# Performance work log

Hardware: AMD Instinct MI355X
Metric: run time of the kernel (lower is better)

The kernel has to match this reference:

```python
import jax, jax.numpy as jnp
import numpy as np

B, T, E = 4, 2048, 1024
H = 16
HS = E // H  # head_size = d_model // num_heads, d_model == E here
D_FF = 4 * E
EPS = 1e-5


def _layernorm(x, g, b):
    mu = jnp.mean(x, axis=-1, keepdims=True)
    var = jnp.var(x, axis=-1, keepdims=True)
    return (x - mu) * jax.lax.rsqrt(var + EPS) * g + b


def setup_inputs() -> dict:
    key = jax.random.key(0)
    ks = jax.random.split(key, 12)
    s_e = 1.0 / np.sqrt(E)
    s_ff = 1.0 / np.sqrt(D_FF)
    return {
        "x": jax.random.normal(ks[0], (B, T, E), jnp.float32),
        "ln1_g": jnp.ones((E,), jnp.float32),
        "ln1_b": jnp.zeros((E,), jnp.float32),
        "Wq": jax.random.normal(ks[1], (E, E), jnp.float32) * s_e,
        "bq": jnp.zeros((E,), jnp.float32),
        "Wk": jax.random.normal(ks[2], (E, E), jnp.float32) * s_e,
        "bk": jnp.zeros((E,), jnp.float32),
        "Wv": jax.random.normal(ks[3], (E, E), jnp.float32) * s_e,
        "bv": jnp.zeros((E,), jnp.float32),
        "Wp": jax.random.normal(ks[4], (E, E), jnp.float32) * s_e,
        "bp": jnp.zeros((E,), jnp.float32),
        "ln2_g": jnp.ones((E,), jnp.float32),
        "ln2_b": jnp.zeros((E,), jnp.float32),
        "W1": jax.random.normal(ks[5], (E, D_FF), jnp.float32) * s_e,
        "b1": jnp.zeros((D_FF,), jnp.float32),
        "W2": jax.random.normal(ks[6], (D_FF, E), jnp.float32) * s_ff,
        "b2": jnp.zeros((E,), jnp.float32),
    }


def reference(x, ln1_g, ln1_b, Wq, bq, Wk, bk, Wv, bv, Wp, bp,
              ln2_g, ln2_b, W1, b1, W2, b2):
    # --- attention sublayer ---
    h = _layernorm(x, ln1_g, ln1_b)                      # [B,T,E]
    q = (h @ Wq + bq).reshape(B, T, H, HS)
    k = (h @ Wk + bk).reshape(B, T, H, HS)
    v = (h @ Wv + bv).reshape(B, T, H, HS)
    scores = jnp.einsum('bqhd,bkhd->bhqk', q, k) * (HS ** -0.5)  # [B,H,T,T]
    causal = jnp.tril(jnp.ones((T, T), bool))
    scores = jnp.where(causal, scores, -jnp.inf)
    w = jax.nn.softmax(scores, axis=-1)
    attn = jnp.einsum('bhqk,bkhd->bqhd', w, v).reshape(B, T, H * HS)
    x = x + attn @ Wp + bp
    # --- FFN sublayer ---
    h2 = _layernorm(x, ln2_g, ln2_b)
    x = x + jax.nn.relu(h2 @ W1 + b1) @ W2 + b2
    return x
```

## Files before the change

kernel.cpp:

```cpp
#include <hip/hip_runtime.h>
#include <hip/hip_bf16.h>

#define B_ 4
#define T_ 2048
#define E_ 1024
#define H_ 16
#define HS_ 64
#define DFF_ 4096
#define M_ (B_ * T_)
#define LDQ_ (3 * E_)

typedef __bf16 bf16_t;
typedef __bf16 bf16x4 __attribute__((ext_vector_type(4)));
typedef __bf16 bf16x8 __attribute__((ext_vector_type(8)));
typedef float f32x4 __attribute__((ext_vector_type(4)));

#define AS1 __attribute__((address_space(1)))
#define AS3 __attribute__((address_space(3)))

__device__ __forceinline__ void gload_lds16(const void* g, void* l) {
  __builtin_amdgcn_global_load_lds((AS1 void*)(g), (AS3 void*)(l), 16, 0, 0);
}

__global__ __launch_bounds__(256) void wtrans_kernel(
    const float* __restrict__ W, bf16_t* __restrict__ Wt, int Krows, int Ncols) {
  __shared__ float tile[32][33];
  int tx = threadIdx.x, ty = threadIdx.y;
  int n0 = blockIdx.x * 32, k0 = blockIdx.y * 32;
#pragma unroll
  for (int i = 0; i < 32; i += 8)
    tile[ty + i][tx] = W[(long)(k0 + ty + i) * Ncols + n0 + tx];
  __syncthreads();
#pragma unroll
  for (int i = 0; i < 32; i += 8)
    Wt[(long)(n0 + ty + i) * Krows + k0 + tx] = (bf16_t)tile[tx][ty + i];
}

__global__ __launch_bounds__(256) void bcat_kernel(const float* a, const float* b,
                                                   const float* c, float* o) {
  int i = blockIdx.x * 256 + threadIdx.x;
  o[i] = i < 1024 ? a[i] : (i < 2048 ? b[i - 1024] : c[i - 2048]);
}

__global__ __launch_bounds__(256) void layernorm_kernel(
    const float* __restrict__ in, const float* __restrict__ g,
    const float* __restrict__ b, bf16_t* __restrict__ out) {
  int row = blockIdx.x;
  int tid = threadIdx.x;
  const float4* inr = (const float4*)(in + (long)row * E_);
  float4 v = inr[tid];
  float s = v.x + v.y + v.z + v.w;
  float ss = v.x * v.x + v.y * v.y + v.z * v.z + v.w * v.w;
#pragma unroll
  for (int o = 32; o; o >>= 1) {
    s += __shfl_xor(s, o);
    ss += __shfl_xor(ss, o);
  }
  __shared__ float red[8];
  int wv = tid >> 6;
  if ((tid & 63) == 0) {
    red[wv] = s;
    red[4 + wv] = ss;
  }
  __syncthreads();
  s = red[0] + red[1] + red[2] + red[3];
  ss = red[4] + red[5] + red[6] + red[7];
  float mu = s * (1.f / E_);
  float var = ss * (1.f / E_) - mu * mu;
  float rs = rsqrtf(var + 1e-5f);
  int ci = tid * 4;
  float4 gv = *(const float4*)(g + ci);
  float4 bv = *(const float4*)(b + ci);
  long o0 = (long)row * E_ + ci;
  out[o0 + 0] = (bf16_t)((v.x - mu) * rs * gv.x + bv.x);
  out[o0 + 1] = (bf16_t)((v.y - mu) * rs * gv.y + bv.y);
  out[o0 + 2] = (bf16_t)((v.z - mu) * rs * gv.z + bv.z);
  out[o0 + 3] = (bf16_t)((v.w - mu) * rs * gv.w + bv.w);
}

template <int MODE>
__global__ __launch_bounds__(256, 2) void gemm_bt_kernel(
    const bf16_t* __restrict__ A, const bf16_t* __restrict__ Bt,
    const float* __restrict__ bias, const float* __restrict__ resid,
    void* __restrict__ out, int N, int K) {
  __shared__ bf16_t As[2][128 * 64];
  __shared__ bf16_t Bs[2][128 * 64];
  const int tid = threadIdx.x;
  const int lane = tid & 63;
  const int wave = tid >> 6;
  const int wr = wave >> 1, wc = wave & 1;
  const int quad = lane >> 4, l16 = lane & 15;
  const int id = blockIdx.y * gridDim.x + blockIdx.x;
  const int xcd = id & 7;
  const int k_ = id >> 3;
  const int bxr = k_ % gridDim.x;
  const int byr = (k_ / gridDim.x) * 8 + xcd;
  const long rowBase = (long)byr * 128;
  const long colBase = (long)bxr * 128;

  f32x4 acc[4][4] = {};

  auto stage = [&](int buf, int k0) {
#pragma unroll
    for (int i = 0; i < 4; ++i) {
      int c = i * 256 + tid;
      int row = c >> 3;
      int gcol = ((c & 7) ^ (row & 7)) * 8;
      gload_lds16(&A[(rowBase + row) * K + k0 + gcol],
                  &As[buf][(i * 256 + wave * 64) * 8]);
      gload_lds16(&Bt[(colBase + row) * K + k0 + gcol],
                  &Bs[buf][(i * 256 + wave * 64) * 8]);
    }
  };

  stage(0, 0);
  __syncthreads();

  for (int k0 = 0; k0 < K; k0 += 64) {
    const int cur = (k0 >> 6) & 1;
    if (k0 + 64 < K) stage(cur ^ 1, k0 + 64);
#pragma unroll
    for (int kk = 0; kk < 2; ++kk) {
      bf16x8 af[4], bfr[4];
#pragma unroll
      for (int i = 0; i < 4; ++i) {
        int rowA = wr * 64 + i * 16 + l16;
        af[i] = *(const bf16x8*)&As[cur][(rowA * 8 + ((quad + 4 * kk) ^ (rowA & 7))) * 8];
        int rowB = wc * 64 + i * 16 + l16;
        bfr[i] = *(const bf16x8*)&Bs[cur][(rowB * 8 + ((quad + 4 * kk) ^ (rowB & 7))) * 8];
      }
#pragma unroll
      for (int mi = 0; mi < 4; ++mi)
#pragma unroll
        for (int ni = 0; ni < 4; ++ni)
          acc[mi][ni] = __builtin_amdgcn_mfma_f32_16x16x32_bf16(
              af[mi], bfr[ni], acc[mi][ni], 0, 0, 0);
    }
    __syncthreads();
  }

#pragma unroll
  for (int mi = 0; mi < 4; ++mi) {
#pragma unroll
    for (int ni = 0; ni < 4; ++ni) {
      int colg = (int)colBase + wc * 64 + ni * 16 + l16;
      float bv = bias[colg];
#pragma unroll
      for (int r = 0; r < 4; ++r) {
        long rowg = rowBase + wr * 64 + mi * 16 + quad * 4 + r;
        float v = acc[mi][ni][r] + bv;
        long idx = rowg * N + colg;
        if (MODE == 0) {
          ((bf16_t*)out)[idx] = (bf16_t)v;
        } else if (MODE == 1) {
          ((float*)out)[idx] = v + resid[idx];
        } else {
          ((bf16_t*)out)[idx] = (bf16_t)fmaxf(v, 0.f);
        }
      }
    }
  }
}

__global__ __launch_bounds__(256) void vtrans_kernel(
    const bf16_t* __restrict__ qkv, bf16_t* __restrict__ vt) {
  __shared__ bf16_t tile[32][33];
  int tx = threadIdx.x, ty = threadIdx.y;
  int t0 = blockIdx.x * 32;
  int d0 = (blockIdx.y & 1) * 32;
  int bh = blockIdx.y >> 1;
  int b = bh >> 4, hh = bh & 15;
#pragma unroll
  for (int i = 0; i < 32; i += 8)
    tile[ty + i][tx] =
        qkv[(long)(b * T_ + t0 + ty + i) * LDQ_ + 2 * E_ + hh * HS_ + d0 + tx];
  __syncthreads();
#pragma unroll
  for (int i = 0; i < 32; i += 8)
    vt[((long)bh * HS_ + d0 + ty + i) * T_ + t0 + tx] = tile[tx][ty + i];
}

__global__ __launch_bounds__(256) void flash_attn_kernel(
    const bf16_t* __restrict__ qkv, const bf16_t* __restrict__ vt,
    bf16_t* __restrict__ attn, bf16_t* __restrict__ Opart,
    float* __restrict__ mlpart) {
  int gx = blockIdx.x;
  int ti = 0, sp = 0;
  for (int t = 0; t < 16; ++t) {
    int ns = t / 6 + 1;
    if (gx < ns) { ti = t; sp = gx; break; }
    gx -= ns;
  }
  const int nsplit = ti / 6 + 1;
  const int totIt = 2 * (ti + 1);
  const int jbeg = 12 * sp;
  const int jend = min(jbeg + 12, totIt);

  const int tid = threadIdx.x;
  const int lane = tid & 63, wave = tid >> 6;
  const int quad = lane >> 4, l16 = lane & 15;
  const int bh = blockIdx.y, b = bh >> 4, hh = bh & 15;
  const int q0 = ti * 128;
  const int qw = q0 + wave * 32;

  __shared__ __align__(16) bf16_t Ks[64][72];
  __shared__ __align__(16) bf16_t Vs[64][72];
  __shared__ __align__(16) bf16_t Ps[4][16][72];

  const bf16_t* qb = qkv;
  const bf16_t* kb = qkv + E_;

  bf16x8 aq[2][2];
#pragma unroll
  for (int s = 0; s < 2; ++s) {
    long base = (long)(b * T_ + qw + s * 16 + l16) * LDQ_ + hh * HS_ + quad * 8;
    aq[s][0] = *(const bf16x8*)&qb[base];
    aq[s][1] = *(const bf16x8*)&qb[base + 32];
#pragma unroll
    for (int e = 0; e < 8; ++e) {
      aq[s][0][e] = (bf16_t)((float)aq[s][0][e] * 0.125f);
      aq[s][1][e] = (bf16_t)((float)aq[s][1][e] * 0.125f);
    }
  }

  f32x4 o[2][4] = {};
  float lsum[2] = {};

  const int srow = tid >> 3;
  const int scol = (tid & 7) * 8;

  for (int j = jbeg; j < jend; ++j) {
    int kv0 = j * 64;
#pragma unroll
    for (int p = 0; p < 2; ++p) {
      int row = p * 32 + srow;
      *(uint4*)&Ks[row][scol] =
          *(const uint4*)&kb[(long)(b * T_ + kv0 + row) * LDQ_ + hh * HS_ + scol];
      *(uint4*)&Vs[row][scol] =
          *(const uint4*)&vt[((long)bh * HS_ + row) * T_ + kv0 + scol];
    }
    __syncthreads();

#pragma unroll
    for (int s = 0; s < 2; ++s) {
      int qs = qw + s * 16;
      if (kv0 <= qs + 15) {
        f32x4 sc[4];
#pragma unroll
        for (int sub = 0; sub < 4; ++sub) {
          f32x4 t = {};
          t = __builtin_amdgcn_mfma_f32_16x16x32_bf16(
              *(const bf16x8*)&Ks[sub * 16 + l16][quad * 8], aq[s][0], t, 0, 0, 0);
          t = __builtin_amdgcn_mfma_f32_16x16x32_bf16(
              *(const bf16x8*)&Ks[sub * 16 + l16][32 + quad * 8], aq[s][1], t, 0, 0, 0);
          sc[sub] = t;
        }
        if (kv0 + 63 > qs) {
          int qcol = qs + l16;
#pragma unroll
          for (int sub = 0; sub < 4; ++sub)
#pragma unroll
            for (int r = 0; r < 4; ++r) {
              int kvrow = kv0 + sub * 16 + quad * 4 + r;
              if (kvrow > qcol) sc[sub][r] = -INFINITY;
            }
        }
        float part = 0.f;
#pragma unroll
        for (int sub = 0; sub < 4; ++sub) {
#pragma unroll
          for (int r = 0; r < 4; ++r) sc[sub][r] = __expf(sc[sub][r]);
          part += (sc[sub][0] + sc[sub][1]) + (sc[sub][2] + sc[sub][3]);
        }
        lsum[s] += part;
#pragma unroll
        for (int sub = 0; sub < 4; ++sub) {
          bf16x4 pk;
#pragma unroll
          for (int r = 0; r < 4; ++r) pk[r] = (bf16_t)sc[sub][r];
          *(bf16x4*)&Ps[wave][l16][sub * 16 + quad * 4] = pk;
        }
        bf16x8 ap0 = *(const bf16x8*)&Ps[wave][l16][quad * 8];
        bf16x8 ap1 = *(const bf16x8*)&Ps[wave][l16][32 + quad * 8];
#pragma unroll
        for (int nt = 0; nt < 4; ++nt) {
          o[s][nt] = __builtin_amdgcn_mfma_f32_16x16x32_bf16(
              *(const bf16x8*)&Vs[nt * 16 + l16][quad * 8], ap0, o[s][nt], 0, 0, 0);
          o[s][nt] = __builtin_amdgcn_mfma_f32_16x16x32_bf16(
              *(const bf16x8*)&Vs[nt * 16 + l16][32 + quad * 8], ap1, o[s][nt], 0, 0, 0);
        }
      }
    }
    __syncthreads();
  }

  float lval[2];
#pragma unroll
  for (int s = 0; s < 2; ++s) {
    float v = lsum[s];
    v += __shfl_xor(v, 16);
    v += __shfl_xor(v, 32);
    lval[s] = v;
  }

  if (nsplit == 1) {
#pragma unroll
    for (int s = 0; s < 2; ++s) {
      float inv = 1.f / lval[s];
      long rowg = (long)b * T_ + qw + s * 16 + l16;
#pragma unroll
      for (int nt = 0; nt < 4; ++nt) {
        bf16x4 pk;
#pragma unroll
        for (int r = 0; r < 4; ++r) pk[r] = (bf16_t)(o[s][nt][r] * inv);
        *(bf16x4*)&attn[rowg * E_ + hh * HS_ + nt * 16 + quad * 4] = pk;
      }
    }
  } else {
    int idx = (ti < 12) ? (ti - 6) * 2 + sp : 12 + (ti - 12) * 3 + sp;
    long slot = (long)bh * 24 + idx;
    bf16_t* op = Opart + slot * (128 * 64);
    float* ml = mlpart + slot * 256;
#pragma unroll
    for (int s = 0; s < 2; ++s) {
      float inv = 1.f / lval[s];
      int rloc = wave * 32 + s * 16 + l16;
#pragma unroll
      for (int nt = 0; nt < 4; ++nt) {
        bf16x4 pk;
#pragma unroll
        for (int r = 0; r < 4; ++r) pk[r] = (bf16_t)(o[s][nt][r] * inv);
        *(bf16x4*)&op[rloc * 64 + nt * 16 + quad * 4] = pk;
      }
      if (quad == 0) ml[rloc] = lval[s];
    }
  }
}

__global__ __launch_bounds__(256) void flash_merge_kernel(
    const bf16_t* __restrict__ Opart, const float* __restrict__ mlpart,
    bf16_t* __restrict__ attn) {
  int ti = 6 + blockIdx.x;
  int bh = blockIdx.y, b = bh >> 4, hh = bh & 15;
  int ns = ti / 6 + 1;
  int base_idx = (ti < 12) ? (ti - 6) * 2 : 12 + (ti - 12) * 3;
  int r = threadIdx.x >> 1;
  int dh = (threadIdx.x & 1) * 32;

  float w[3], den = 0.f;
  for (int s = 0; s < ns; ++s) {
    long slot = (long)bh * 24 + base_idx + s;
    w[s] = mlpart[slot * 256 + r];
    den += w[s];
  }
  float inv = 1.f / den;
  float acc[32];
#pragma unroll
  for (int d = 0; d < 32; ++d) acc[d] = 0.f;
  for (int s = 0; s < ns; ++s) {
    long slot = (long)bh * 24 + base_idx + s;
    const bf16_t* op = Opart + slot * (128 * 64) + r * 64 + dh;
#pragma unroll
    for (int d = 0; d < 32; ++d) acc[d] += w[s] * (float)op[d];
  }
  long rowg = (long)b * T_ + ti * 128 + r;
  bf16_t* dst = attn + rowg * E_ + hh * HS_ + dh;
#pragma unroll
  for (int d = 0; d < 32; ++d) dst[d] = (bf16_t)(acc[d] * inv);
}

extern "C" void kernel_launch(void* const* d_in, const int* in_sizes, int n_in,
                              void* d_out, int out_size, void* d_ws,
                              size_t ws_size, hipStream_t stream) {
  const float* x = (const float*)d_in[0];
  const float* ln1_g = (const float*)d_in[1];
  const float* ln1_b = (const float*)d_in[2];
  const float* Wq = (const float*)d_in[3];
  const float* bq = (const float*)d_in[4];
  const float* Wk = (const float*)d_in[5];
  const float* bk = (const float*)d_in[6];
  const float* Wv = (const float*)d_in[7];
  const float* bv = (const float*)d_in[8];
  const float* Wp = (const float*)d_in[9];
  const float* bp = (const float*)d_in[10];
  const float* ln2_g = (const float*)d_in[11];
  const float* ln2_b = (const float*)d_in[12];
  const float* W1 = (const float*)d_in[13];
  const float* b1 = (const float*)d_in[14];
  const float* W2 = (const float*)d_in[15];
  const float* b2 = (const float*)d_in[16];
  float* out = (float*)d_out;

  const size_t MB = 1ull << 20;
  char* ws = (char*)d_ws;
  bf16_t* wqkvt = (bf16_t*)(ws + 0 * MB);
  bf16_t* wpt   = (bf16_t*)(ws + 6 * MB);
  bf16_t* w1t   = (bf16_t*)(ws + 8 * MB);
  bf16_t* w2t   = (bf16_t*)(ws + 16 * MB);
  float*  bqkv  = (float*)(ws + 24 * MB);
  bf16_t* h     = (bf16_t*)(ws + 25 * MB);
  bf16_t* qkvb  = (bf16_t*)(ws + 41 * MB);
  bf16_t* vt    = (bf16_t*)(ws + 89 * MB);
  float*  xmid  = (float*)(ws + 105 * MB);
  bf16_t* Opart = (bf16_t*)(ws + 105 * MB);
  float* mlpart = (float*)(ws + 131 * MB);
  bf16_t* attn  = h;
  bf16_t* h2    = h;
  bf16_t* ff1   = qkvb;

  dim3 tb(32, 8);
  wtrans_kernel<<<dim3(E_ / 32, E_ / 32), tb, 0, stream>>>(Wq, wqkvt, E_, E_);
  wtrans_kernel<<<dim3(E_ / 32, E_ / 32), tb, 0, stream>>>(Wk, wqkvt + (long)E_ * E_, E_, E_);
  wtrans_kernel<<<dim3(E_ / 32, E_ / 32), tb, 0, stream>>>(Wv, wqkvt + 2l * E_ * E_, E_, E_);
  wtrans_kernel<<<dim3(E_ / 32, E_ / 32), tb, 0, stream>>>(Wp, wpt, E_, E_);
  wtrans_kernel<<<dim3(DFF_ / 32, E_ / 32), tb, 0, stream>>>(W1, w1t, E_, DFF_);
  wtrans_kernel<<<dim3(E_ / 32, DFF_ / 32), tb, 0, stream>>>(W2, w2t, DFF_, E_);
  bcat_kernel<<<12, 256, 0, stream>>>(bq, bk, bv, bqkv);

  layernorm_kernel<<<M_, 256, 0, stream>>>(x, ln1_g, ln1_b, h);

  gemm_bt_kernel<0><<<dim3(3 * E_ / 128, M_ / 128), 256, 0, stream>>>(
      h, wqkvt, bqkv, nullptr, qkvb, 3 * E_, E_);

  vtrans_kernel<<<dim3(T_ / 32, 2 * B_ * H_), tb, 0, stream>>>(qkvb, vt);

  flash_attn_kernel<<<dim3(30, B_ * H_), 256, 0, stream>>>(qkvb, vt, attn,
                                                           Opart, mlpart);
  flash_merge_kernel<<<dim3(10, B_ * H_), 256, 0, stream>>>(Opart, mlpart, attn);

  gemm_bt_kernel<1><<<dim3(E_ / 128, M_ / 128), 256, 0, stream>>>(
      attn, wpt, bp, x, xmid, E_, E_);

  layernorm_kernel<<<M_, 256, 0, stream>>>(xmid, ln2_g, ln2_b, h2);

  gemm_bt_kernel<2><<<dim3(DFF_ / 128, M_ / 128), 256, 0, stream>>>(
      h2, w1t, b1, nullptr, ff1, DFF_, E_);
  gemm_bt_kernel<1><<<dim3(E_ / 128, M_ / 128), 256, 0, stream>>>(
      ff1, w2t, b2, xmid, out, E_, DFF_);
}
```

Baseline: 523.9 us.

## Double-buffer K/V tiles via async global-to-LDS loads with XOR-swizzled layout

```diff
diff --git a/kernel.cpp b/kernel.cpp
--- a/kernel.cpp
+++ b/kernel.cpp
@@ -203,9 +203,9 @@
   const int q0 = ti * 128;
   const int qw = q0 + wave * 32;
 
-  __shared__ __align__(16) bf16_t Ks[64][72];
-  __shared__ __align__(16) bf16_t Vs[64][72];
-  __shared__ __align__(16) bf16_t Ps[4][16][72];
+  __shared__ __align__(16) bf16_t Ks[2][64 * 64];
+  __shared__ __align__(16) bf16_t Vs[2][64 * 64];
+  __shared__ __align__(16) bf16_t Ps[4][16 * 64];
 
   const bf16_t* qb = qkv;
   const bf16_t* kb = qkv + E_;
@@ -226,35 +226,49 @@
   f32x4 o[2][4] = {};
   float lsum[2] = {};
 
-  const int srow = tid >> 3;
-  const int scol = (tid & 7) * 8;
+  auto stage = [&](int buf, int j) {
+    const int kv0 = j * 64;
+#pragma unroll
+    for (int i = 0; i < 2; ++i) {
+      int c = i * 256 + tid;
+      int row = c >> 3;
+      int gcol = ((c & 7) ^ (row & 7)) * 8;
+      gload_lds16(&kb[(long)(b * T_ + kv0 + row) * LDQ_ + hh * HS_ + gcol],
+                  &Ks[buf][(i * 256 + wave * 64) * 8]);
+      gload_lds16(&vt[((long)bh * HS_ + row) * T_ + kv0 + gcol],
+                  &Vs[buf][(i * 256 + wave * 64) * 8]);
+    }
+  };
+
+  stage(0, jbeg);
+  __syncthreads();
 
   for (int j = jbeg; j < jend; ++j) {
-    int kv0 = j * 64;
-#pragma unroll
-    for (int p = 0; p < 2; ++p) {
-      int row = p * 32 + srow;
-      *(uint4*)&Ks[row][scol] =
-          *(const uint4*)&kb[(long)(b * T_ + kv0 + row) * LDQ_ + hh * HS_ + scol];
-      *(uint4*)&Vs[row][scol] =
-          *(const uint4*)&vt[((long)bh * HS_ + row) * T_ + kv0 + scol];
-    }
-    __syncthreads();
+    const int kv0 = j * 64;
+    const int cur = (j - jbeg) & 1;
+    if (j + 1 < jend) stage(cur ^ 1, j + 1);
+    const bf16_t* KsL = Ks[cur];
+    const bf16_t* VsL = Vs[cur];
+    bf16_t* Pw = Ps[wave];
 
 #pragma unroll
     for (int s = 0; s < 2; ++s) {
-      int qs = qw + s * 16;
+      const int qs = qw + s * 16;
       if (kv0 <= qs + 15) {
         f32x4 sc[4];
+        __builtin_amdgcn_s_setprio(1);
 #pragma unroll
         for (int sub = 0; sub < 4; ++sub) {
+          const int rk = sub * 16 + l16;
+          const int k0 = rk * 64 + ((quad ^ (rk & 7)) * 8);
           f32x4 t = {};
           t = __builtin_amdgcn_mfma_f32_16x16x32_bf16(
-              *(const bf16x8*)&Ks[sub * 16 + l16][quad * 8], aq[s][0], t, 0, 0, 0);
+              *(const bf16x8*)&KsL[k0], aq[s][0], t, 0, 0, 0);
           t = __builtin_amdgcn_mfma_f32_16x16x32_bf16(
-              *(const bf16x8*)&Ks[sub * 16 + l16][32 + quad * 8], aq[s][1], t, 0, 0, 0);
+              *(const bf16x8*)&KsL[k0 ^ 32], aq[s][1], t, 0, 0, 0);
           sc[sub] = t;
         }
+        __builtin_amdgcn_s_setprio(0);
         if (kv0 + 63 > qs) {
           int qcol = qs + l16;
 #pragma unroll
@@ -278,17 +292,24 @@
           bf16x4 pk;
 #pragma unroll
           for (int r = 0; r < 4; ++r) pk[r] = (bf16_t)sc[sub][r];
-          *(bf16x4*)&Ps[wave][l16][sub * 16 + quad * 4] = pk;
-        }
-        bf16x8 ap0 = *(const bf16x8*)&Ps[wave][l16][quad * 8];
-        bf16x8 ap1 = *(const bf16x8*)&Ps[wave][l16][32 + quad * 8];
+          const int ch = sub * 2 + (quad >> 1);
+          const int off = ((ch ^ (l16 & 7)) * 8) + ((quad & 1) * 4);
+          *(bf16x4*)&Pw[l16 * 64 + off] = pk;
+        }
+        const int p0 = l16 * 64 + ((quad ^ (l16 & 7)) * 8);
+        bf16x8 ap0 = *(const bf16x8*)&Pw[p0];
+        bf16x8 ap1 = *(const bf16x8*)&Pw[p0 ^ 32];
+        __builtin_amdgcn_s_setprio(1);
 #pragma unroll
         for (int nt = 0; nt < 4; ++nt) {
+          const int rv = nt * 16 + l16;
+          const int v0 = rv * 64 + ((quad ^ (rv & 7)) * 8);
           o[s][nt] = __builtin_amdgcn_mfma_f32_16x16x32_bf16(
-              *(const bf16x8*)&Vs[nt * 16 + l16][quad * 8], ap0, o[s][nt], 0, 0, 0);
+              *(const bf16x8*)&VsL[v0], ap0, o[s][nt], 0, 0, 0);
           o[s][nt] = __builtin_amdgcn_mfma_f32_16x16x32_bf16(
-              *(const bf16x8*)&Vs[nt * 16 + l16][32 + quad * 8], ap1, o[s][nt], 0, 0, 0);
-        }
+              *(const bf16x8*)&VsL[v0 ^ 32], ap1, o[s][nt], 0, 0, 0);
+        }
+        __builtin_amdgcn_s_setprio(0);
       }
     }
     __syncthreads();
```

After: 508.6 us. 1.03x faster.
